# Optimization experiments

Hardware: AMD Instinct MI355X
Metric: run time of the kernel (lower is better)

Reference implementation:

```python
import jax, jax.numpy as jnp
import numpy as np

D_MODEL = 1024
N_HEADS = 16
D_K = D_MODEL // N_HEADS
FF_DIM = 4096
EPS = 1e-6
NEG = -1.0e9


def _layernorm(x, g, b):
    # torch: a_2 * (x - mean) / (std + eps) + b_2, std is unbiased (ddof=1)
    mean = jnp.mean(x, axis=-1, keepdims=True)
    std = jnp.std(x, axis=-1, keepdims=True, ddof=1)
    return g * (x - mean) / (std + EPS) + b


def setup_inputs() -> dict:
    key = jax.random.key(0)
    ks = jax.random.split(key, 8)
    s = 0.02
    x = jax.random.normal(ks[0], (2, 2048, D_MODEL), dtype=jnp.float32)
    mask = jnp.ones((2, 1, 1, 2048), dtype=jnp.int32)
    return {
        "x": x,
        "mask": mask,
        "wq": jax.random.normal(ks[1], (D_MODEL, D_MODEL), jnp.float32) * s,
        "wk": jax.random.normal(ks[2], (D_MODEL, D_MODEL), jnp.float32) * s,
        "wv": jax.random.normal(ks[3], (D_MODEL, D_MODEL), jnp.float32) * s,
        "wo": jax.random.normal(ks[4], (D_MODEL, D_MODEL), jnp.float32) * s,
        "bq": jnp.zeros((D_MODEL,), jnp.float32),
        "bk": jnp.zeros((D_MODEL,), jnp.float32),
        "bv": jnp.zeros((D_MODEL,), jnp.float32),
        "bo": jnp.zeros((D_MODEL,), jnp.float32),
        "w1": jax.random.normal(ks[5], (D_MODEL, FF_DIM), jnp.float32) * s,
        "b1": jnp.zeros((FF_DIM,), jnp.float32),
        "w2": jax.random.normal(ks[6], (FF_DIM, D_MODEL), jnp.float32) * s,
        "b2": jnp.zeros((D_MODEL,), jnp.float32),
        "ln1_g": jnp.ones((D_MODEL,), jnp.float32),
        "ln1_b": jnp.zeros((D_MODEL,), jnp.float32),
        "ln2_g": jnp.ones((D_MODEL,), jnp.float32),
        "ln2_b": jnp.zeros((D_MODEL,), jnp.float32),
    }


def reference(x, mask, wq, wk, wv, wo, bq, bk, bv, bo, w1, b1, w2, b2,
              ln1_g, ln1_b, ln2_g, ln2_b):
    B, S, _ = x.shape
    # --- sublayer 1: pre-norm self-attention with residual ---
    h = _layernorm(x, ln1_g, ln1_b)
    q = (h @ wq + bq).reshape(B, S, N_HEADS, D_K).transpose(0, 2, 1, 3)
    k = (h @ wk + bk).reshape(B, S, N_HEADS, D_K).transpose(0, 2, 1, 3)
    v = (h @ wv + bv).reshape(B, S, N_HEADS, D_K).transpose(0, 2, 1, 3)
    scores = jnp.einsum('bhqd,bhkd->bhqk', q, k) / np.sqrt(D_K).astype(np.float32)
    scores = jnp.where(mask == 0, NEG, scores)
    attn = jax.nn.softmax(scores, axis=-1)
    ctx = jnp.einsum('bhqk,bhkd->bhqd', attn, v)
    ctx = ctx.transpose(0, 2, 1, 3).reshape(B, S, D_MODEL)
    x = x + (ctx @ wo + bo)
    # --- sublayer 2: pre-norm FFN with residual ---
    h2 = _layernorm(x, ln2_g, ln2_b)
    ff = jax.nn.relu(h2 @ w1 + b1) @ w2 + b2
    return x + ff
```

## Files before the change

kernel.cpp:

```cpp
#include <hip/hip_runtime.h>

typedef unsigned short u16;
typedef unsigned int u32;
typedef __attribute__((ext_vector_type(8))) short bf16x8;
typedef __attribute__((ext_vector_type(4))) float f32x4;

__device__ __forceinline__ u16 f2bf(float f) {
  union { float f; unsigned int u; } x;
  x.f = f;
  unsigned int r = x.u + 0x7fffu + ((x.u >> 16) & 1u);
  return (u16)(r >> 16);
}

__device__ __forceinline__ float bf2f(u16 v) {
  union { unsigned int u; float f; } x;
  x.u = ((unsigned int)v) << 16;
  return x.f;
}

__device__ __forceinline__ u32 fbits(float f) {
  union { float f; u32 u; } x; x.f = f; return x.u;
}

__device__ __forceinline__ void async16(const u16* g, u16* l) {
  __builtin_amdgcn_global_load_lds((const __attribute__((address_space(1))) void*)g,
                                   (__attribute__((address_space(3))) void*)l, 16, 0, 0);
}

__device__ __forceinline__ void stage128x64(const u16* __restrict__ src, long row0, int k0,
                                            int ld, u16* lds, int wave, int lane) {
#pragma unroll
  for (int r = 0; r < 4; ++r) {
    int s = r * 256 + wave * 64 + lane;
    int row = s >> 3;
    int c = (s & 7) ^ (row & 7);
    async16(src + (row0 + row) * (long)ld + k0 + c * 8, lds + (r * 256 + wave * 64) * 8);
  }
}

__device__ __forceinline__ void stage_half512(const u16* __restrict__ src, long row0, int k0,
                                              int ld, u16* lbase, int wave, int lane) {
#pragma unroll
  for (int r = 0; r < 2; ++r) {
    int s = r * 512 + wave * 64 + lane;
    int row = s >> 3;
    int c = (s & 7) ^ (row & 7);
    async16(src + (row0 + row) * (long)ld + k0 + c * 8, lbase + (r * 512 + wave * 64) * 8);
  }
}

__device__ __forceinline__ void stage64x128(const u16* __restrict__ src, int col0, int ld,
                                            u16* lds, int wave, int lane) {
#pragma unroll
  for (int r = 0; r < 4; ++r) {
    int s = r * 256 + wave * 64 + lane;
    int row = s >> 4;
    int c = (s & 15) ^ (row & 15);
    async16(src + (long)row * ld + col0 + c * 8, lds + (r * 256 + wave * 64) * 8);
  }
}

__device__ __forceinline__ void ln_core(float4 v, const float* g, const float* b, int t,
                                        u16* outrow) {
  float s = v.x + v.y + v.z + v.w;
  float ss = v.x * v.x + v.y * v.y + v.z * v.z + v.w * v.w;
#pragma unroll
  for (int off = 32; off; off >>= 1) {
    s += __shfl_xor(s, off);
    ss += __shfl_xor(ss, off);
  }
  __shared__ float red[8];
  int wave = t >> 6, lane = t & 63;
  if (lane == 0) { red[wave] = s; red[wave + 4] = ss; }
  __syncthreads();
  float tot = red[0] + red[1] + red[2] + red[3];
  float tots = red[4] + red[5] + red[6] + red[7];
  float mean = tot * (1.0f / 1024.0f);
  float var = (tots - 1024.0f * mean * mean) * (1.0f / 1023.0f);
  var = fmaxf(var, 0.0f);
  float inv = 1.0f / (sqrtf(var) + 1e-6f);
  float4 gv = ((const float4*)g)[t];
  float4 bv = ((const float4*)b)[t];
  union { unsigned long long u64; u16 h[4]; } o;
  o.h[0] = f2bf(gv.x * (v.x - mean) * inv + bv.x);
  o.h[1] = f2bf(gv.y * (v.y - mean) * inv + bv.y);
  o.h[2] = f2bf(gv.z * (v.z - mean) * inv + bv.z);
  o.h[3] = f2bf(gv.w * (v.w - mean) * inv + bv.w);
  *(unsigned long long*)(outrow + t * 4) = o.u64;
}

__global__ __launch_bounds__(256) void prep(const float* __restrict__ wq,
                                            const float* __restrict__ wk,
                                            const float* __restrict__ wv,
                                            const float* __restrict__ wo,
                                            const float* __restrict__ w1,
                                            const float* __restrict__ w2,
                                            const float* __restrict__ x,
                                            const float* __restrict__ ln1_g,
                                            const float* __restrict__ ln1_b,
                                            u16* __restrict__ wqkvT,
                                            u16* __restrict__ w1T,
                                            u16* __restrict__ w2T,
                                            u16* __restrict__ hout) {
  const int bid = blockIdx.x;
  const int part = bid >> 12;
  const int local = bid & 4095;
  const int t = threadIdx.x;
  if (part == 1) {
    float4 v = ((const float4*)(x + (long)local * 1024))[t];
    ln_core(v, ln1_g, ln1_b, t, hout + (long)local * 1024);
    return;
  }
  __shared__ float tile[32][33];
  const float* src; u16* dst; int C, R, bx, by;
  if (part == 0) {
    int sub = local >> 10;
    src = sub == 0 ? wq : (sub == 1 ? wk : (sub == 2 ? wv : wo));
    dst = wqkvT + (long)sub * 1024 * 1024;
    C = 1024; R = 1024; bx = local & 31; by = (local >> 5) & 31;
  } else if (part == 2) {
    src = w1; dst = w1T; C = 4096; R = 1024; bx = local & 127; by = local >> 7;
  } else {
    src = w2; dst = w2T; C = 1024; R = 4096; bx = local & 31; by = local >> 5;
  }
  int c0 = bx * 32, r0 = by * 32;
  int tx = t & 31, ty = t >> 5;
#pragma unroll
  for (int i = 0; i < 32; i += 8)
    tile[ty + i][tx] = src[(long)(r0 + ty + i) * C + c0 + tx];
  __syncthreads();
#pragma unroll
  for (int i = 0; i < 32; i += 8)
    dst[(long)(c0 + ty + i) * R + r0 + tx] = f2bf(tile[tx][ty + i]);
}

__global__ __launch_bounds__(256) void ln_fuse(const float* x, const float* bres,
                                               const u16* p0, const u16* p1,
                                               const u16* p2, const u16* p3,
                                               const float* g, const float* b,
                                               float* yout, u16* hout) {
  int row = blockIdx.x, t = threadIdx.x;
  long base = (long)row * 1024;
  float4 xv = ((const float4*)(x + base))[t];
  float4 bo = ((const float4*)bres)[t];
  ushort4 a = ((const ushort4*)(p0 + base))[t];
  ushort4 c = ((const ushort4*)(p1 + base))[t];
  ushort4 d = ((const ushort4*)(p2 + base))[t];
  ushort4 e = ((const ushort4*)(p3 + base))[t];
  float4 y;
  y.x = xv.x + bo.x + (bf2f(a.x) + bf2f(c.x)) + (bf2f(d.x) + bf2f(e.x));
  y.y = xv.y + bo.y + (bf2f(a.y) + bf2f(c.y)) + (bf2f(d.y) + bf2f(e.y));
  y.z = xv.z + bo.z + (bf2f(a.z) + bf2f(c.z)) + (bf2f(d.z) + bf2f(e.z));
  y.w = xv.w + bo.w + (bf2f(a.w) + bf2f(c.w)) + (bf2f(d.w) + bf2f(e.w));
  ((float4*)(yout + base))[t] = y;
  ln_core(y, g, b, t, hout + base);
}

__global__ __launch_bounds__(256) void final_add(float* __restrict__ out,
                                                 const float* __restrict__ b2,
                                                 const u16* __restrict__ p0,
                                                 const u16* __restrict__ p1,
                                                 const u16* __restrict__ p2) {
  int row = blockIdx.x, t = threadIdx.x;
  long base = (long)row * 1024;
  float4 o = ((float4*)(out + base))[t];
  float4 bb = ((const float4*)b2)[t];
  ushort4 a = ((const ushort4*)(p0 + base))[t];
  ushort4 c = ((const ushort4*)(p1 + base))[t];
  ushort4 d = ((const ushort4*)(p2 + base))[t];
  o.x += bb.x + (bf2f(a.x) + bf2f(c.x)) + bf2f(d.x);
  o.y += bb.y + (bf2f(a.y) + bf2f(c.y)) + bf2f(d.y);
  o.z += bb.z + (bf2f(a.z) + bf2f(c.z)) + bf2f(d.z);
  o.w += bb.w + (bf2f(a.w) + bf2f(c.w)) + bf2f(d.w);
  ((float4*)(out + base))[t] = o;
}

template <int MODE, int SWZ>
__global__ __launch_bounds__(512, 1) void gemm8(const u16* __restrict__ A,
                                                const u16* __restrict__ Bt, int M, int N, int K,
                                                void* __restrict__ outp,
                                                const float* __restrict__ bias,
                                                const float* __restrict__ bias1,
                                                const float* __restrict__ bias2,
                                                u16* __restrict__ q_out, u16* __restrict__ k_out,
                                                u16* __restrict__ v_out) {
  __shared__ __align__(16) u16 lds[65536];
  (void)M;
  const int tid = threadIdx.x;
  const int wave = tid >> 6, lane = tid & 63;
  const int lane16 = lane & 15, quad = lane >> 4;
  const int wr2 = wave >> 2, wc2 = wave & 3;
  int bx = blockIdx.x, by = blockIdx.y;
  if (SWZ) {
    const int fid = by * gridDim.x + bx;
    const int xcd = fid & 7, slot = fid >> 3;
    const int nxh = gridDim.x >> 1;
    bx = (xcd & 1) * nxh + slot % nxh;
    by = (xcd >> 1) * 4 + slot / nxh;
  }
  const long m0 = (long)by * 256;
  const long n0 = (long)bx * 256;
  const int kLen = K / gridDim.z;
  const int kBeg = blockIdx.z * kLen;
  const int nT = kLen >> 6;

  u16* const ldsA = lds;
  u16* const ldsB = lds + 32768;

  const f32x4 fzero = {0.f, 0.f, 0.f, 0.f};
  f32x4 acc[2][2][4][2];
#pragma unroll
  for (int qa = 0; qa < 2; ++qa)
#pragma unroll
    for (int qb = 0; qb < 2; ++qb)
#pragma unroll
      for (int m = 0; m < 4; ++m)
#pragma unroll
        for (int n = 0; n < 2; ++n) acc[qa][qb][m][n] = fzero;

  stage_half512(A,  m0,       kBeg,      K, ldsA,                 wave, lane);
  stage_half512(Bt, n0,       kBeg,      K, ldsB,                 wave, lane);
  stage_half512(Bt, n0 + 128, kBeg,      K, ldsB + 8192,          wave, lane);
  stage_half512(A,  m0 + 128, kBeg,      K, ldsA + 8192,          wave, lane);
  stage_half512(A,  m0,       kBeg + 64, K, ldsA + 16384,         wave, lane);
  stage_half512(Bt, n0,       kBeg + 64, K, ldsB + 16384,         wave, lane);
  stage_half512(Bt, n0 + 128, kBeg + 64, K, ldsB + 16384 + 8192,  wave, lane);
  asm volatile("s_waitcnt vmcnt(10)" ::: "memory");
  asm volatile("s_barrier" ::: "memory");

  for (int t = 0; t < nT; ++t) {
    u16* const aB = ldsA + (t & 1) * 16384;
    u16* const bB = ldsB + (t & 1) * 16384;
    u16* const aN1 = ldsA + ((t + 1) & 1) * 16384;
    const int k1 = kBeg + (t + 1 < nT ? t + 1 : nT - 1) * 64;
    const int k2 = kBeg + (t + 2 < nT ? t + 2 : nT - 1) * 64;

    bf16x8 af[4][2], b0f[2][2], b1f[2][2];

#pragma unroll
    for (int m = 0; m < 4; ++m) {
      const int row = wr2 * 64 + m * 16 + lane16;
#pragma unroll
      for (int kk = 0; kk < 2; ++kk)
        af[m][kk] = *(const bf16x8*)(aB + row * 64 + (((kk * 4 + quad) ^ (row & 7)) << 3));
    }
#pragma unroll
    for (int n = 0; n < 2; ++n) {
      const int row = wc2 * 32 + n * 16 + lane16;
#pragma unroll
      for (int kk = 0; kk < 2; ++kk)
        b0f[n][kk] = *(const bf16x8*)(bB + row * 64 + (((kk * 4 + quad) ^ (row & 7)) << 3));
    }
    stage_half512(A, m0 + 128, k1, K, aN1 + 8192, wave, lane);
    asm volatile("s_barrier" ::: "memory");
    asm volatile("s_waitcnt lgkmcnt(0)" ::: "memory");
    __builtin_amdgcn_sched_barrier(0);
    __builtin_amdgcn_s_setprio(1);
#pragma unroll
    for (int m = 0; m < 4; ++m)
#pragma unroll
      for (int n = 0; n < 2; ++n) {
        acc[0][0][m][n] = __builtin_amdgcn_mfma_f32_16x16x32_bf16(af[m][0], b0f[n][0], acc[0][0][m][n], 0, 0, 0);
        acc[0][0][m][n] = __builtin_amdgcn_mfma_f32_16x16x32_bf16(af[m][1], b0f[n][1], acc[0][0][m][n], 0, 0, 0);
      }
    __builtin_amdgcn_s_setprio(0);
    asm volatile("s_waitcnt vmcnt(10)" ::: "memory");
    asm volatile("s_barrier" ::: "memory");

#pragma unroll
    for (int n = 0; n < 2; ++n) {
      const int row = 128 + wc2 * 32 + n * 16 + lane16;
#pragma unroll
      for (int kk = 0; kk < 2; ++kk)
        b1f[n][kk] = *(const bf16x8*)(bB + row * 64 + (((kk * 4 + quad) ^ (row & 7)) << 3));
    }
    stage_half512(A, m0, k2, K, aB, wave, lane);
    asm volatile("s_barrier" ::: "memory");
    asm volatile("s_waitcnt lgkmcnt(0)" ::: "memory");
    __builtin_amdgcn_sched_barrier(0);
    __builtin_amdgcn_s_setprio(1);
#pragma unroll
    for (int m = 0; m < 4; ++m)
#pragma unroll
      for (int n = 0; n < 2; ++n) {
        acc[0][1][m][n] = __builtin_amdgcn_mfma_f32_16x16x32_bf16(af[m][0], b1f[n][0], acc[0][1][m][n], 0, 0, 0);
        acc[0][1][m][n] = __builtin_amdgcn_mfma_f32_16x16x32_bf16(af[m][1], b1f[n][1], acc[0][1][m][n], 0, 0, 0);
      }
    __builtin_amdgcn_s_setprio(0);
    asm volatile("s_waitcnt vmcnt(10)" ::: "memory");
    asm volatile("s_barrier" ::: "memory");

#pragma unroll
    for (int m = 0; m < 4; ++m) {
      const int row = 128 + wr2 * 64 + m * 16 + lane16;
#pragma unroll
      for (int kk = 0; kk < 2; ++kk)
        af[m][kk] = *(const bf16x8*)(aB + row * 64 + (((kk * 4 + quad) ^ (row & 7)) << 3));
    }
    stage_half512(Bt, n0, k2, K, bB, wave, lane);
    asm volatile("s_barrier" ::: "memory");
    asm volatile("s_waitcnt lgkmcnt(0)" ::: "memory");
    __builtin_amdgcn_sched_barrier(0);
    __builtin_amdgcn_s_setprio(1);
#pragma unroll
    for (int m = 0; m < 4; ++m)
#pragma unroll
      for (int n = 0; n < 2; ++n) {
        acc[1][1][m][n] = __builtin_amdgcn_mfma_f32_16x16x32_bf16(af[m][0], b1f[n][0], acc[1][1][m][n], 0, 0, 0);
        acc[1][1][m][n] = __builtin_amdgcn_mfma_f32_16x16x32_bf16(af[m][1], b1f[n][1], acc[1][1][m][n], 0, 0, 0);
      }
    __builtin_amdgcn_s_setprio(0);
    asm volatile("s_waitcnt vmcnt(10)" ::: "memory");
    asm volatile("s_barrier" ::: "memory");

    stage_half512(Bt, n0 + 128, k2, K, bB + 8192, wave, lane);
    asm volatile("s_barrier" ::: "memory");
    __builtin_amdgcn_s_setprio(1);
#pragma unroll
    for (int m = 0; m < 4; ++m)
#pragma unroll
      for (int n = 0; n < 2; ++n) {
        acc[1][0][m][n] = __builtin_amdgcn_mfma_f32_16x16x32_bf16(af[m][0], b0f[n][0], acc[1][0][m][n], 0, 0, 0);
        acc[1][0][m][n] = __builtin_amdgcn_mfma_f32_16x16x32_bf16(af[m][1], b0f[n][1], acc[1][0][m][n], 0, 0, 0);
      }
    __builtin_amdgcn_s_setprio(0);
    asm volatile("s_waitcnt vmcnt(10)" ::: "memory");
    asm volatile("s_barrier" ::: "memory");
  }

  asm volatile("s_waitcnt vmcnt(0)" ::: "memory");

  if (MODE == 0) {
    const int sel = (int)(n0 >> 10);
    if (sel == 2) {
#pragma unroll
      for (int qa = 0; qa < 2; ++qa)
#pragma unroll
        for (int qb = 0; qb < 2; ++qb) {
          __syncthreads();
#pragma unroll
          for (int n = 0; n < 2; ++n) {
            const int lcol = wc2 * 32 + n * 16 + lane16;
            const float bvj = bias2[(int)(n0 - 2048) + qb * 128 + lcol];
#pragma unroll
            for (int m = 0; m < 4; ++m)
#pragma unroll
              for (int r = 0; r < 4; ++r) {
                const int lrow = wr2 * 64 + m * 16 + quad * 4 + r;
                lds[lcol * 136 + lrow] = f2bf(acc[qa][qb][m][n][r] + bvj);
              }
          }
          __syncthreads();
          const int lcol = tid >> 2, seg = tid & 3;
          const int cc = (int)(n0 - 2048) + qb * 128 + lcol;
          const int head = cc >> 6, d = cc & 63;
          const int bI = (int)((m0 + qa * 128) >> 11);
          const int s0 = (int)((m0 + qa * 128) & 2047);
          u16* dst = v_out + ((long)(bI * 16 + head) * 64 + d) * 2048 + s0 + seg * 32;
          const u16* s = lds + lcol * 136 + seg * 32;
#pragma unroll
          for (int c2 = 0; c2 < 4; ++c2) ((uint4*)dst)[c2] = ((const uint4*)s)[c2];
        }
      return;
    }
    u16* qk = sel == 0 ? q_out : k_out;
    const float* bb = sel == 0 ? bias : bias1;
#pragma unroll
    for (int qa = 0; qa < 2; ++qa)
#pragma unroll
      for (int qb = 0; qb < 2; ++qb)
#pragma unroll
        for (int n = 0; n < 2; ++n) {
          const int col = (int)n0 + qb * 128 + wc2 * 32 + n * 16 + lane16;
          const int cc = col & 1023;
          const float bv = bb[cc];
          const int head = cc >> 6, d = cc & 63;
#pragma unroll
          for (int m = 0; m < 4; ++m) {
            const int rw = (int)m0 + qa * 128 + wr2 * 64 + m * 16 + quad * 4;
#pragma unroll
            for (int r = 0; r < 4; ++r) {
              const int row = rw + r;
              const int bI = row >> 11, sS = row & 2047;
              const long bh = (long)bI * 16 + head;
              float vv = acc[qa][qb][m][n][r] + bv;
              if (sel == 0) vv *= 0.18033688f;
              qk[(bh * 2048 + sS) * 64 + d] = f2bf(vv);
            }
          }
        }
  } else if (MODE == 2) {
    u16* op = (u16*)outp;
#pragma unroll
    for (int qa = 0; qa < 2; ++qa)
#pragma unroll
      for (int qb = 0; qb < 2; ++qb)
#pragma unroll
        for (int n = 0; n < 2; ++n) {
          const int col = (int)n0 + qb * 128 + wc2 * 32 + n * 16 + lane16;
          const float bv = bias[col];
#pragma unroll
          for (int m = 0; m < 4; ++m) {
            const long rbase = ((long)m0 + qa * 128 + wr2 * 64 + m * 16 + quad * 4) * N + col;
#pragma unroll
            for (int r = 0; r < 4; ++r)
              op[rbase + (long)r * N] = f2bf(fmaxf(acc[qa][qb][m][n][r] + bv, 0.0f));
          }
        }
  } else {
    const int z = blockIdx.z;
    if (MODE == 3 && z == 3) {
      float* op = (float*)v_out;
#pragma unroll
      for (int qa = 0; qa < 2; ++qa)
#pragma unroll
        for (int qb = 0; qb < 2; ++qb)
#pragma unroll
          for (int n = 0; n < 2; ++n) {
            const int col = (int)n0 + qb * 128 + wc2 * 32 + n * 16 + lane16;
#pragma unroll
            for (int m = 0; m < 4; ++m) {
              const long rbase = ((long)m0 + qa * 128 + wr2 * 64 + m * 16 + quad * 4) * N + col;
#pragma unroll
              for (int r = 0; r < 4; ++r)
                unsafeAtomicAdd(op + rbase + (long)r * N, acc[qa][qb][m][n][r]);
            }
          }
    } else {
      u16* pp = z == 0 ? (u16*)outp : (z == 1 ? q_out : (z == 2 ? k_out : v_out));
#pragma unroll
      for (int qa = 0; qa < 2; ++qa)
#pragma unroll
        for (int qb = 0; qb < 2; ++qb)
#pragma unroll
          for (int n = 0; n < 2; ++n) {
            const int col = (int)n0 + qb * 128 + wc2 * 32 + n * 16 + lane16;
#pragma unroll
            for (int m = 0; m < 4; ++m) {
              const long rbase = ((long)m0 + qa * 128 + wr2 * 64 + m * 16 + quad * 4) * N + col;
#pragma unroll
              for (int r = 0; r < 4; ++r)
                pp[rbase + (long)r * N] = f2bf(acc[qa][qb][m][n][r]);
            }
          }
    }
  }
}

#define FA_C0 28.854239f
__global__ __launch_bounds__(256) void flash_attn(const u16* __restrict__ q,
                                                  const u16* __restrict__ k,
                                                  const u16* __restrict__ v,
                                                  const int* __restrict__ mask,
                                                  u16* __restrict__ ctx) {
  const int fid = blockIdx.y * 16 + blockIdx.x;
  const int xcd = fid & 7, slot = fid >> 3;
  const int bh = xcd * 4 + (slot >> 4);
  const int q0 = (slot & 15) * 128;
  const int b = bh >> 4, h = bh & 15;
  const int tid = threadIdx.x;
  const int wave = tid >> 6, lane = tid & 63;
  const int lane16 = lane & 15, quad = lane >> 4;

  const u16* qp = q + (long)bh * 2048 * 64;
  const u16* kp = k + (long)bh * 2048 * 64;
  const u16* vp = v + (long)bh * 64 * 2048;
  const int* mp = mask + b * 2048;

  __shared__ __align__(16) u16 ldsK[128 * 64];
  __shared__ __align__(16) u16 ldsVT[64 * 128];
  __shared__ __align__(16) u16 ldsP23[2 * 4096];
  __shared__ int ldsFlag[16];
  u16* myP = (wave < 2) ? (ldsK + wave * 4096) : (ldsP23 + (wave - 2) * 4096);

  {
    int4 ma = ((const int4*)mp)[tid * 2];
    int4 mb = ((const int4*)mp)[tid * 2 + 1];
    bool ok = ma.x && ma.y && ma.z && ma.w && mb.x && mb.y && mb.z && mb.w;
    unsigned long long bal = __ballot(ok);
    if ((lane & 15) == 0) {
      int i = lane >> 4;
      ldsFlag[wave * 4 + i] = (((bal >> (16 * i)) & 0xFFFFull) == 0xFFFFull) ? 1 : 0;
    }
  }

  bf16x8 qf[2][2];
#pragma unroll
  for (int g = 0; g < 2; ++g) {
    const long qrow = q0 + wave * 32 + g * 16 + lane16;
    qf[g][0] = *(const bf16x8*)(qp + qrow * 64 + quad * 8);
    qf[g][1] = *(const bf16x8*)(qp + qrow * 64 + 32 + quad * 8);
  }

  const f32x4 fzero = {0.f, 0.f, 0.f, 0.f};
  const f32x4 cC0 = {-FA_C0, -FA_C0, -FA_C0, -FA_C0};
  float l_loc[2] = {0.f, 0.f};
  f32x4 o_acc[2][4];
#pragma unroll
  for (int g = 0; g < 2; ++g)
#pragma unroll
    for (int j = 0; j < 4; ++j) o_acc[g][j] = fzero;

  const int xorm = (lane16 & 7) << 2;
  u16* const pw0 = myP + lane16 * 128;
  u16* const pw1 = myP + (16 + lane16) * 128;

  stage128x64(kp, 0, 0, 64, ldsK, wave, lane);
  stage64x128(vp, 0, 2048, ldsVT, wave, lane);
  __syncthreads();

  for (int kt = 0; kt < 2048; kt += 128) {
    const int ktn = (kt + 128 < 2048) ? kt + 128 : kt;

    uint4 krg[4], vrg[4];
#pragma unroll
    for (int r = 0; r < 4; ++r) {
      int s = r * 256 + wave * 64 + lane;
      int row = s >> 3, c = (s & 7) ^ (row & 7);
      krg[r] = *(const uint4*)(kp + (long)(ktn + row) * 64 + c * 8);
    }
#pragma unroll
    for (int r = 0; r < 4; ++r) {
      int s = r * 256 + wave * 64 + lane;
      int row = s >> 4, c = (s & 15) ^ (row & 15);
      vrg[r] = *(const uint4*)(vp + (long)row * 2048 + ktn + c * 8);
    }
    const bool allv = ldsFlag[kt >> 7] != 0;

    f32x4 s_acc[8][2];
    __builtin_amdgcn_s_setprio(1);
#pragma unroll
    for (int j = 0; j < 8; ++j) {
      int row = j * 16 + lane16;
      int c0i = quad ^ (row & 7);
      int c1i = (4 + quad) ^ (row & 7);
      bf16x8 kf0 = *(const bf16x8*)(ldsK + row * 64 + c0i * 8);
      bf16x8 kf1 = *(const bf16x8*)(ldsK + row * 64 + c1i * 8);
#pragma unroll
      for (int g = 0; g < 2; ++g) {
        f32x4 sa = __builtin_amdgcn_mfma_f32_16x16x32_bf16(kf0, qf[g][0], cC0, 0, 0, 0);
        sa = __builtin_amdgcn_mfma_f32_16x16x32_bf16(kf1, qf[g][1], sa, 0, 0, 0);
        s_acc[j][g] = sa;
      }
    }
    __builtin_amdgcn_s_setprio(0);
    __syncthreads();

#pragma unroll
    for (int j = 0; j < 8; ++j) {
      int cw = ((4 * j + quad) ^ xorm) * 4;
      f32x4 mk = fzero;
      if (!allv) {
        int4 mi = *(const int4*)(mp + kt + j * 16 + quad * 4);
        mk[0] = (mi.x == 0) ? -1.0e9f : 0.0f;
        mk[1] = (mi.y == 0) ? -1.0e9f : 0.0f;
        mk[2] = (mi.z == 0) ? -1.0e9f : 0.0f;
        mk[3] = (mi.w == 0) ? -1.0e9f : 0.0f;
      }
#pragma unroll
      for (int g = 0; g < 2; ++g) {
        f32x4 sa = s_acc[j][g];
        if (!allv) sa = sa + mk;
        float p0 = __builtin_exp2f(sa[0]);
        float p1 = __builtin_exp2f(sa[1]);
        float p2 = __builtin_exp2f(sa[2]);
        float p3 = __builtin_exp2f(sa[3]);
        l_loc[g] += (p0 + p1) + (p2 + p3);
        uint2 pk;
        pk.x = __builtin_amdgcn_perm(fbits(p1), fbits(p0), 0x07060302u);
        pk.y = __builtin_amdgcn_perm(fbits(p3), fbits(p2), 0x07060302u);
        *(uint2*)((g ? pw1 : pw0) + cw) = pk;
      }
    }
    __builtin_amdgcn_s_setprio(1);
#pragma unroll
    for (int kk = 0; kk < 4; ++kk) {
      int cr = ((8 * kk + 2 * quad) ^ xorm) * 4;
      bf16x8 pf0 = *(const bf16x8*)(pw0 + cr);
      bf16x8 pf1 = *(const bf16x8*)(pw1 + cr);
#pragma unroll
      for (int jj = 0; jj < 4; ++jj) {
        int row = jj * 16 + lane16;
        int cv = (kk * 4 + quad) ^ (row & 15);
        bf16x8 vf = *(const bf16x8*)(ldsVT + row * 128 + cv * 8);
        o_acc[0][jj] = __builtin_amdgcn_mfma_f32_16x16x32_bf16(pf0, vf, o_acc[0][jj], 0, 0, 0);
        o_acc[1][jj] = __builtin_amdgcn_mfma_f32_16x16x32_bf16(pf1, vf, o_acc[1][jj], 0, 0, 0);
      }
    }
    __builtin_amdgcn_s_setprio(0);

    asm volatile("s_waitcnt vmcnt(0)" ::: "memory");
    asm volatile("s_barrier" ::: "memory");
#pragma unroll
    for (int r = 0; r < 4; ++r) {
      int s = r * 256 + wave * 64 + lane;
      *(uint4*)(ldsK + s * 8) = krg[r];
    }
#pragma unroll
    for (int r = 0; r < 4; ++r) {
      int s = r * 256 + wave * 64 + lane;
      *(uint4*)(ldsVT + s * 8) = vrg[r];
    }
    __syncthreads();
  }

  float lr[2][4];
#pragma unroll
  for (int g = 0; g < 2; ++g) {
    float l = l_loc[g];
#pragma unroll
    for (int off = 16; off < 64; off <<= 1) l += __shfl_xor(l, off);
    float linv = 1.0f / l;
#pragma unroll
    for (int r = 0; r < 4; ++r) lr[g][r] = __shfl(linv, quad * 4 + r);
  }

#pragma unroll
  for (int g = 0; g < 2; ++g)
#pragma unroll
    for (int jj = 0; jj < 4; ++jj)
#pragma unroll
      for (int r = 0; r < 4; ++r) {
        int sg = q0 + wave * 32 + g * 16 + quad * 4 + r;
        int d = jj * 16 + lane16;
        float val = o_acc[g][jj][r] * lr[g][r];
        ctx[((long)b * 2048 + sg) * 1024 + h * 64 + d] = f2bf(val);
      }
}

extern "C" void kernel_launch(void* const* d_in, const int* in_sizes, int n_in, void* d_out,
                              int out_size, void* d_ws, size_t ws_size, hipStream_t stream) {
  (void)in_sizes; (void)n_in; (void)out_size; (void)ws_size;
  const float* x  = (const float*)d_in[0];
  const int* mask = (const int*)d_in[1];
  const float* wq = (const float*)d_in[2];
  const float* wk = (const float*)d_in[3];
  const float* wv = (const float*)d_in[4];
  const float* wo = (const float*)d_in[5];
  const float* bq = (const float*)d_in[6];
  const float* bk = (const float*)d_in[7];
  const float* bv = (const float*)d_in[8];
  const float* bo = (const float*)d_in[9];
  const float* w1 = (const float*)d_in[10];
  const float* b1 = (const float*)d_in[11];
  const float* w2 = (const float*)d_in[12];
  const float* b2 = (const float*)d_in[13];
  const float* ln1_g = (const float*)d_in[14];
  const float* ln1_b = (const float*)d_in[15];
  const float* ln2_g = (const float*)d_in[16];
  const float* ln2_b = (const float*)d_in[17];
  float* out = (float*)d_out;

  u16* ws = (u16*)d_ws;
  u16* wqkvT = ws;
  u16* woT = wqkvT + 3072 * 1024;
  u16* w1T = woT + 1024 * 1024;
  u16* w2T = w1T + 4096 * 1024;
  u16* h   = w2T + 4096 * 1024;
  u16* qb  = h + 4096 * 1024;
  u16* kb  = qb + 4096 * 1024;
  u16* vb  = kb + 4096 * 1024;
  u16* ctx = vb + 4096 * 1024;
  u16* ffh = qb;

  prep<<<16384, 256, 0, stream>>>(wq, wk, wv, wo, w1, w2, x, ln1_g, ln1_b,
                                  wqkvT, w1T, w2T, h);

  gemm8<0, 1><<<dim3(12, 16), 512, 0, stream>>>(h, wqkvT, 4096, 3072, 1024, nullptr,
                                                bq, bk, bv, qb, kb, vb);

  flash_attn<<<dim3(16, 32), 256, 0, stream>>>(qb, kb, vb, mask, ctx);

  gemm8<1, 0><<<dim3(4, 16, 4), 512, 0, stream>>>(ctx, woT, 4096, 1024, 1024, h,
                                                  nullptr, nullptr, nullptr, qb, kb, vb);

  ln_fuse<<<4096, 256, 0, stream>>>(x, bo, h, qb, kb, vb, ln2_g, ln2_b, out, h);

  gemm8<2, 1><<<dim3(16, 16), 512, 0, stream>>>(h, w1T, 4096, 4096, 1024, ffh, b1,
                                                nullptr, nullptr, nullptr, nullptr, nullptr);

  gemm8<3, 0><<<dim3(4, 16, 4), 512, 0, stream>>>(ffh, w2T, 4096, 1024, 4096, ws,
                                                  nullptr, nullptr, nullptr, w1T, h, (u16*)out);

  final_add<<<4096, 256, 0, stream>>>(out, b2, ws, w1T, h);
}
```

Baseline: 392.7 us.

## Double-buffer K/V tiles in LDS with async staging in attention kernel

The attention kernel previously prefetched the next K/V tile into registers and copied it into a single LDS buffer after each iteration. It now keeps two LDS buffers for K and V^T and issues async global-to-LDS staging for the next tile into the alternate buffer at the start of each iteration. This removes the register round-trip, the per-iteration LDS store phase and one barrier. In exchange LDS use per block goes up, which may lower occupancy. The P scratch for waves 0-1 now aliases the current K buffer.

```diff
diff --git a/kernel.cpp b/kernel.cpp
--- a/kernel.cpp
+++ b/kernel.cpp
@@ -467,11 +467,10 @@
   const u16* vp = v + (long)bh * 64 * 2048;
   const int* mp = mask + b * 2048;
 
-  __shared__ __align__(16) u16 ldsK[128 * 64];
-  __shared__ __align__(16) u16 ldsVT[64 * 128];
+  __shared__ __align__(16) u16 ldsK[2][128 * 64];
+  __shared__ __align__(16) u16 ldsVT[2][64 * 128];
   __shared__ __align__(16) u16 ldsP23[2 * 4096];
   __shared__ int ldsFlag[16];
-  u16* myP = (wave < 2) ? (ldsK + wave * 4096) : (ldsP23 + (wave - 2) * 4096);
 
   {
     int4 ma = ((const int4*)mp)[tid * 2];
@@ -502,29 +501,22 @@
     for (int j = 0; j < 4; ++j) o_acc[g][j] = fzero;
 
   const int xorm = (lane16 & 7) << 2;
-  u16* const pw0 = myP + lane16 * 128;
-  u16* const pw1 = myP + (16 + lane16) * 128;
-
-  stage128x64(kp, 0, 0, 64, ldsK, wave, lane);
-  stage64x128(vp, 0, 2048, ldsVT, wave, lane);
+
+  stage128x64(kp, 0, 0, 64, ldsK[0], wave, lane);
+  stage64x128(vp, 0, 2048, ldsVT[0], wave, lane);
   __syncthreads();
 
   for (int kt = 0; kt < 2048; kt += 128) {
-    const int ktn = (kt + 128 < 2048) ? kt + 128 : kt;
-
-    uint4 krg[4], vrg[4];
-#pragma unroll
-    for (int r = 0; r < 4; ++r) {
-      int s = r * 256 + wave * 64 + lane;
-      int row = s >> 3, c = (s & 7) ^ (row & 7);
-      krg[r] = *(const uint4*)(kp + (long)(ktn + row) * 64 + c * 8);
-    }
-#pragma unroll
-    for (int r = 0; r < 4; ++r) {
-      int s = r * 256 + wave * 64 + lane;
-      int row = s >> 4, c = (s & 15) ^ (row & 15);
-      vrg[r] = *(const uint4*)(vp + (long)row * 2048 + ktn + c * 8);
-    }
+    const int cb = (kt >> 7) & 1;
+    u16* const curK = ldsK[cb];
+    u16* const curVT = ldsVT[cb];
+    if (kt + 128 < 2048) {
+      stage128x64(kp, kt + 128, 0, 64, ldsK[cb ^ 1], wave, lane);
+      stage64x128(vp, kt + 128, 2048, ldsVT[cb ^ 1], wave, lane);
+    }
+    u16* const myP = (wave < 2) ? (curK + wave * 4096) : (ldsP23 + (wave - 2) * 4096);
+    u16* const pw0 = myP + lane16 * 128;
+    u16* const pw1 = myP + (16 + lane16) * 128;
     const bool allv = ldsFlag[kt >> 7] != 0;
 
     f32x4 s_acc[8][2];
@@ -534,8 +526,8 @@
       int row = j * 16 + lane16;
       int c0i = quad ^ (row & 7);
       int c1i = (4 + quad) ^ (row & 7);
-      bf16x8 kf0 = *(const bf16x8*)(ldsK + row * 64 + c0i * 8);
-      bf16x8 kf1 = *(const bf16x8*)(ldsK + row * 64 + c1i * 8);
+      bf16x8 kf0 = *(const bf16x8*)(curK + row * 64 + c0i * 8);
+      bf16x8 kf1 = *(const bf16x8*)(curK + row * 64 + c1i * 8);
 #pragma unroll
       for (int g = 0; g < 2; ++g) {
         f32x4 sa = __builtin_amdgcn_mfma_f32_16x16x32_bf16(kf0, qf[g][0], cC0, 0, 0, 0);
@@ -544,7 +536,7 @@
       }
     }
     __builtin_amdgcn_s_setprio(0);
-    __syncthreads();
+    asm volatile("s_barrier" ::: "memory");
 
 #pragma unroll
     for (int j = 0; j < 8; ++j) {
@@ -582,7 +574,7 @@
       for (int jj = 0; jj < 4; ++jj) {
         int row = jj * 16 + lane16;
         int cv = (kk * 4 + quad) ^ (row & 15);
-        bf16x8 vf = *(const bf16x8*)(ldsVT + row * 128 + cv * 8);
+        bf16x8 vf = *(const bf16x8*)(curVT + row * 128 + cv * 8);
         o_acc[0][jj] = __builtin_amdgcn_mfma_f32_16x16x32_bf16(pf0, vf, o_acc[0][jj], 0, 0, 0);
         o_acc[1][jj] = __builtin_amdgcn_mfma_f32_16x16x32_bf16(pf1, vf, o_acc[1][jj], 0, 0, 0);
       }
@@ -591,17 +583,6 @@
 
     asm volatile("s_waitcnt vmcnt(0)" ::: "memory");
     asm volatile("s_barrier" ::: "memory");
-#pragma unroll
-    for (int r = 0; r < 4; ++r) {
-      int s = r * 256 + wave * 64 + lane;
-      *(uint4*)(ldsK + s * 8) = krg[r];
-    }
-#pragma unroll
-    for (int r = 0; r < 4; ++r) {
-      int s = r * 256 + wave * 64 + lane;
-      *(uint4*)(ldsVT + s * 8) = vrg[r];
-    }
-    __syncthreads();
   }
 
   float lr[2][4];
```

After: 396.0 us. Within noise of the previous version (+0.8%).
